# Optimization experiments

Measured on AMD Instinct MI355X. Metric: run time of the kernel, lower is better.

## Reference

```python
import jax, jax.numpy as jnp
import numpy as np

N, FIN, NH, NR, F, E = 50000, 256, 4, 4, 64, 500000


def setup_inputs() -> dict:
    key = jax.random.key(0)
    ks = jax.random.split(key, 12)
    x = jax.random.normal(ks[0], (N, FIN), jnp.float32)
    src = jax.random.randint(ks[1], (E,), 0, N)
    trg = jax.random.randint(ks[2], (E,), 0, N)
    rel = jax.random.randint(ks[3], (E,), 0, NR)
    node_to_graph_map = jnp.zeros((N,), jnp.int32)
    s = 1.0 / np.sqrt(FIN)
    W_proj = jax.random.uniform(ks[4], (NH * NR * F, FIN), jnp.float32, -s, s)
    score_src = jax.random.normal(ks[5], (1, NH, NR, F), jnp.float32) * 0.1
    score_trg = jax.random.normal(ks[6], (1, NH, NR, F), jnp.float32) * 0.1
    sf = 1.0 / np.sqrt(F)
    W1 = jax.random.uniform(ks[7], (F, F), jnp.float32, -sf, sf)
    b1 = jnp.zeros((F,), jnp.float32)
    W2 = jax.random.uniform(ks[8], (F, F), jnp.float32, -sf, sf)
    b2 = jnp.zeros((F,), jnp.float32)
    W3 = jax.random.uniform(ks[9], (1, F), jnp.float32, -sf, sf)
    b3 = jnp.zeros((1,), jnp.float32)
    W_skip = jax.random.uniform(ks[10], (NH * F, FIN), jnp.float32, -s, s)
    bias = jnp.zeros((NH * F,), jnp.float32)
    gamma = jnp.ones((NH * F,), jnp.float32)
    beta = jnp.zeros((NH * F,), jnp.float32)
    return dict(x=x, src=src, trg=trg, rel=rel, node_to_graph_map=node_to_graph_map,
                W_proj=W_proj, score_src=score_src, score_trg=score_trg,
                W1=W1, b1=b1, W2=W2, b2=b2, W3=W3, b3=b3,
                W_skip=W_skip, bias=bias, gamma=gamma, beta=beta)


def mish(v):
    return v * jnp.tanh(jax.nn.softplus(v))


def gat_forward(x, W_proj, score_src, score_trg, W1, b1, W2, b2, W3, b3,
                W_skip, bias, gamma, beta, src, trg, rel):
    n = x.shape[0]
    # (N, NH, NR, F) projected node features
    proj = (x @ W_proj.T).reshape(n, NH, NR, F)
    s_src = (proj * score_src).sum(-1)  # (N, NH, NR)
    s_trg = (proj * score_trg).sum(-1)  # (N, NH, NR)
    # lift to edges for their own relation: (E, NH)
    e_s = s_src[src, :, rel] + s_trg[trg, :, rel]
    e_s = jax.nn.leaky_relu(e_s, 0.2)
    # per-(relation, head) max over edges (matches per-relation max(dim=0) in the torch loop)
    m = jax.ops.segment_max(e_s, rel, num_segments=NR)  # (NR, NH)
    e_exp = jnp.exp(e_s - m[rel])
    # segment softmax grouped by (target node, relation)
    seg = trg * NR + rel
    denom = jax.ops.segment_sum(e_exp, seg, num_segments=n * NR)  # (N*NR, NH)
    att = e_exp / (denom[seg] + 1e-16)  # (E, NH)
    feat = proj[src, :, rel, :] * att[:, :, None]  # (E, NH, F)
    agg = jax.ops.segment_sum(feat, seg, num_segments=n * NR)  # (N*NR, NH, F)
    agg = agg.reshape(n, NR, NH, F).transpose(0, 2, 1, 3)  # (N, NH, NR, F)
    # AttentionedAggregationLayer: MLP score -> Mish -> softmax over relation dim -> weighted sum
    h = jax.nn.relu(agg @ W1.T + b1)
    h = jax.nn.relu(h @ W2.T + b2)
    sc = mish(h @ W3.T + b3)            # (N, NH, NR, 1)
    a_rel = jax.nn.softmax(sc, axis=-2)
    out = (agg * a_rel).sum(-2)          # (N, NH, F)
    # skip connection (FIN != NH*F per-head, so projected skip), concat heads, bias, ELU, LayerNorm
    out = out + (x @ W_skip.T).reshape(n, NH, F)
    out = out.reshape(n, NH * F) + bias
    out = jax.nn.elu(out)
    mu = out.mean(-1, keepdims=True)
    var = out.var(-1, keepdims=True)
    out = (out - mu) * jax.lax.rsqrt(var + 1e-5) * gamma + beta
    return out


def reference(x, src, trg, rel, node_to_graph_map, W_proj, score_src, score_trg,
              W1, b1, W2, b2, W3, b3, W_skip, bias, gamma, beta):
    return gat_forward(x, W_proj, score_src, score_trg, W1, b1, W2, b2, W3, b3,
                       W_skip, bias, gamma, beta, src, trg, rel)
```

## Files before the change

kernel.cpp:

```cpp
#include <hip/hip_runtime.h>

#define NNODES 50000
#define NEDGES 500000
#define NBINS  (NNODES * 4)
#define NSCANB 196
#define MPAD   50176

#define WF_W1    0
#define WF_B1    4096
#define WF_W2    4160
#define WF_B2    8256
#define WF_W3    8320
#define WF_B3    8384
#define WF_SSC   8385
#define WF_STC   9409
#define WF_BIAS  10433
#define WF_GAMMA 10689
#define WF_BETA  10945
#define WF_TOT   11201

typedef __attribute__((ext_vector_type(8))) short short8;
typedef __attribute__((ext_vector_type(4))) short short4v;
typedef __attribute__((ext_vector_type(4))) float floatx4;
typedef __attribute__((ext_vector_type(4))) unsigned int uint4v;

__device__ __forceinline__ float bf2f(unsigned short u) {
    return __uint_as_float(((unsigned)u) << 16);
}
__device__ __forceinline__ unsigned f2bf(float f) {
    unsigned u = __float_as_uint(f);
    u += 0x7fffu + ((u >> 16) & 1u);
    return u >> 16;
}
__device__ __forceinline__ float bflo(unsigned u) { return __uint_as_float(u << 16); }
__device__ __forceinline__ float bfhi(unsigned u) { return __uint_as_float(u & 0xffff0000u); }
__device__ __forceinline__ int clampi(int v, int hi) { return v < 0 ? 0 : (v > hi ? hi : v); }

__device__ __forceinline__ short8 pack_bf16(const float* p) {
    short8 r;
#pragma unroll
    for (int j = 0; j < 8; j++) r[j] = (short)f2bf(p[j]);
    return r;
}

__global__ __launch_bounds__(256) void probe_k(const unsigned short* __restrict__ xs,
                                               unsigned* __restrict__ flag) {
    __shared__ unsigned cnt;
    if (threadIdx.x == 0) cnt = 0;
    __syncthreads();
    unsigned local = 0;
    for (int i = threadIdx.x; i < 8192; i += 256) {
        float v = bf2f(xs[i]);
        if (!(fabsf(v) < 1e10f)) local++;
    }
    atomicAdd(&cnt, local);
    __syncthreads();
    if (threadIdx.x == 0) *flag = (cnt > 256u) ? 1u : 0u;
}

__device__ __forceinline__ float ldf(const void* p, int i, bool f32) {
    return f32 ? ((const float*)p)[i] : bf2f(((const unsigned short*)p)[i]);
}

__global__ __launch_bounds__(1024) void wconv_k(const void* W1, const void* b1,
                                                const void* W2, const void* b2,
                                                const void* W3, const void* b3,
                                                const void* ssc, const void* stc,
                                                const void* bias, const void* gamma,
                                                const void* beta,
                                                const unsigned* __restrict__ flag,
                                                float* __restrict__ wf) {
    bool f32 = (*flag != 0u);
    for (int i = threadIdx.x; i < WF_TOT; i += 1024) {
        float v;
        if (i < WF_B1)          v = ldf(W1, i - WF_W1, f32);
        else if (i < WF_W2)     v = ldf(b1, i - WF_B1, f32);
        else if (i < WF_B2)     v = ldf(W2, i - WF_W2, f32);
        else if (i < WF_W3)     v = ldf(b2, i - WF_B2, f32);
        else if (i < WF_B3)     v = ldf(W3, i - WF_W3, f32);
        else if (i < WF_SSC)    v = ldf(b3, i - WF_B3, f32);
        else if (i < WF_STC)    v = ldf(ssc, i - WF_SSC, f32);
        else if (i < WF_BIAS)   v = ldf(stc, i - WF_STC, f32);
        else if (i < WF_GAMMA)  v = ldf(bias, i - WF_BIAS, f32);
        else if (i < WF_BETA)   v = ldf(gamma, i - WF_GAMMA, f32);
        else                    v = ldf(beta, i - WF_BETA, f32);
        wf[i] = v;
    }
}

__global__ __launch_bounds__(256) void convbf_k(const void* __restrict__ src,
                                                unsigned short* __restrict__ dst,
                                                int nelem, int npad,
                                                const unsigned* __restrict__ flag) {
    int i8 = (blockIdx.x * 256 + threadIdx.x) * 8;
    if (i8 >= npad) return;
    short8 o;
    if (i8 < nelem) {
        if (*flag) {
            const float* pf = (const float*)src + i8;
            floatx4 a = *(const floatx4*)pf;
            floatx4 b = *(const floatx4*)(pf + 4);
            o[0] = (short)f2bf(a[0]); o[1] = (short)f2bf(a[1]);
            o[2] = (short)f2bf(a[2]); o[3] = (short)f2bf(a[3]);
            o[4] = (short)f2bf(b[0]); o[5] = (short)f2bf(b[1]);
            o[6] = (short)f2bf(b[2]); o[7] = (short)f2bf(b[3]);
        } else {
            o = *(const short8*)((const unsigned short*)src + i8);
        }
    } else {
#pragma unroll
        for (int j = 0; j < 8; j++) o[j] = 0;
    }
    *(short8*)(dst + i8) = o;
}

__global__ __launch_bounds__(64) void gemm_fused_k(const unsigned short* __restrict__ A,
                                                   const unsigned short* __restrict__ Bp,
                                                   const unsigned short* __restrict__ Bs,
                                                   unsigned short* __restrict__ proj,
                                                   unsigned short* __restrict__ out16,
                                                   float* __restrict__ out32,
                                                   const float* __restrict__ wf,
                                                   float* __restrict__ s_src,
                                                   float* __restrict__ s_trg,
                                                   const unsigned* __restrict__ flag) {
    const bool cf32 = (*flag != 0u);
    const int lane = threadIdx.x & 63;
    const int l15 = lane & 15, q = lane >> 4;
    const int m0 = blockIdx.x * 64;

    short8 af[4][8];
#pragma unroll
    for (int mt = 0; mt < 4; mt++)
#pragma unroll
        for (int ks = 0; ks < 8; ks++)
            af[mt][ks] = *(const short8*)(A + (size_t)(m0 + mt * 16 + l15) * 256 + ks * 32 + q * 8);

#pragma unroll 1
    for (int cg = 0; cg < 16; cg++) {
        floatx4 acc[4][4];
#pragma unroll
        for (int i = 0; i < 4; i++)
#pragma unroll
            for (int j = 0; j < 4; j++) acc[i][j] = (floatx4){0.f, 0.f, 0.f, 0.f};
#pragma unroll
        for (int ks = 0; ks < 8; ks++) {
            short8 bfr[4];
#pragma unroll
            for (int nt = 0; nt < 4; nt++)
                bfr[nt] = *(const short8*)(Bp + (size_t)(cg * 64 + nt * 16 + l15) * 256 + ks * 32 + q * 8);
#pragma unroll
            for (int mt = 0; mt < 4; mt++)
#pragma unroll
                for (int nt = 0; nt < 4; nt++)
                    acc[mt][nt] = __builtin_amdgcn_mfma_f32_16x16x32_bf16(af[mt][ks], bfr[nt],
                                                                         acc[mt][nt], 0, 0, 0);
        }
        const int h = cg >> 2, r = cg & 3;
        const int colbase = (r * 4 + h) * 64;
        const int cell = h * 4 + r;
        float sa[4], sb[4];
#pragma unroll
        for (int nt = 0; nt < 4; nt++) {
            sa[nt] = wf[WF_SSC + cell * 64 + nt * 16 + l15];
            sb[nt] = wf[WF_STC + cell * 64 + nt * 16 + l15];
        }
#pragma unroll
        for (int mt = 0; mt < 4; mt++) {
            float pa[4] = {0.f, 0.f, 0.f, 0.f};
            float pb[4] = {0.f, 0.f, 0.f, 0.f};
#pragma unroll
            for (int nt = 0; nt < 4; nt++)
#pragma unroll
                for (int rg = 0; rg < 4; rg++) {
                    int row = m0 + mt * 16 + q * 4 + rg;
                    float v = acc[mt][nt][rg];
                    unsigned short vb = (unsigned short)f2bf(v);
                    if (row < NNODES)
                        proj[(size_t)row * 1024 + colbase + nt * 16 + l15] = vb;
                    float vr = bf2f(vb);
                    pa[rg] = fmaf(vr, sa[nt], pa[rg]);
                    pb[rg] = fmaf(vr, sb[nt], pb[rg]);
                }
#pragma unroll
            for (int off = 1; off < 16; off <<= 1)
#pragma unroll
                for (int rg = 0; rg < 4; rg++) {
                    pa[rg] += __shfl_xor(pa[rg], off);
                    pb[rg] += __shfl_xor(pb[rg], off);
                }
            if (l15 == 0) {
#pragma unroll
                for (int rg = 0; rg < 4; rg++) {
                    int row = m0 + mt * 16 + q * 4 + rg;
                    if (row < NNODES) {
                        s_src[row * 16 + cell] = pa[rg];
                        s_trg[row * 16 + cell] = pb[rg];
                    }
                }
            }
        }
    }

#pragma unroll 1
    for (int cg = 0; cg < 4; cg++) {
        floatx4 acc[4][4];
#pragma unroll
        for (int i = 0; i < 4; i++)
#pragma unroll
            for (int j = 0; j < 4; j++) acc[i][j] = (floatx4){0.f, 0.f, 0.f, 0.f};
#pragma unroll
        for (int ks = 0; ks < 8; ks++) {
            short8 bfr[4];
#pragma unroll
            for (int nt = 0; nt < 4; nt++)
                bfr[nt] = *(const short8*)(Bs + (size_t)(cg * 64 + nt * 16 + l15) * 256 + ks * 32 + q * 8);
#pragma unroll
            for (int mt = 0; mt < 4; mt++)
#pragma unroll
                for (int nt = 0; nt < 4; nt++)
                    acc[mt][nt] = __builtin_amdgcn_mfma_f32_16x16x32_bf16(af[mt][ks], bfr[nt],
                                                                         acc[mt][nt], 0, 0, 0);
        }
#pragma unroll
        for (int mt = 0; mt < 4; mt++)
#pragma unroll
            for (int nt = 0; nt < 4; nt++)
#pragma unroll
                for (int rg = 0; rg < 4; rg++) {
                    int row = m0 + mt * 16 + q * 4 + rg;
                    if (row < NNODES) {
                        size_t idx = (size_t)row * 256 + cg * 64 + nt * 16 + l15;
                        float v = acc[mt][nt][rg];
                        if (cf32) out32[idx] = v;
                        else      out16[idx] = (unsigned short)f2bf(v);
                    }
                }
    }
}

__global__ __launch_bounds__(256) void count_k(const int* __restrict__ trg,
                                               const int* __restrict__ rel,
                                               unsigned* __restrict__ counts, int E) {
    int e = blockIdx.x * 256 + threadIdx.x;
    if (e >= E) return;
    int g = clampi(trg[e], NNODES - 1);
    int r = clampi(rel[e], 3);
    atomicAdd(&counts[g * 4 + r], 1u);
}

__global__ __launch_bounds__(256) void scan1_k(const unsigned* __restrict__ counts,
                                               unsigned* __restrict__ offsets,
                                               unsigned* __restrict__ bsum) {
    __shared__ unsigned ts[256];
    int t = threadIdx.x;
    int base = blockIdx.x * 1024 + t * 4;
    uint4v c = {0u, 0u, 0u, 0u};
    if (base + 3 < NBINS) c = *(const uint4v*)(counts + base);
    else {
#pragma unroll
        for (int j = 0; j < 4; j++) c[j] = (base + j < NBINS) ? counts[base + j] : 0u;
    }
    ts[t] = c[0] + c[1] + c[2] + c[3];
    __syncthreads();
    for (int off = 1; off < 256; off <<= 1) {
        unsigned v = (t >= off) ? ts[t - off] : 0u;
        __syncthreads();
        ts[t] += v;
        __syncthreads();
    }
    unsigned pre = (t == 0) ? 0u : ts[t - 1];
    uint4v o;
    o[0] = pre;
    o[1] = pre + c[0];
    o[2] = pre + c[0] + c[1];
    o[3] = pre + c[0] + c[1] + c[2];
    if (base + 3 < NBINS) *(uint4v*)(offsets + base) = o;
    else {
#pragma unroll
        for (int j = 0; j < 4; j++) if (base + j < NBINS) offsets[base + j] = o[j];
    }
    if (t == 255) bsum[blockIdx.x] = ts[255];
}

__global__ __launch_bounds__(256) void scan2_k(unsigned* __restrict__ bsum,
                                               unsigned* __restrict__ offsets) {
    __shared__ unsigned ts[256];
    int t = threadIdx.x;
    unsigned v = (t < NSCANB) ? bsum[t] : 0u;
    ts[t] = v;
    __syncthreads();
    for (int off = 1; off < 256; off <<= 1) {
        unsigned u = (t >= off) ? ts[t - off] : 0u;
        __syncthreads();
        ts[t] += u;
        __syncthreads();
    }
    if (t < NSCANB) bsum[t] = (t == 0) ? 0u : ts[t - 1];
    if (t == 255) offsets[NBINS] = ts[255];
}

__global__ __launch_bounds__(256) void scan3_k(unsigned* __restrict__ offsets,
                                               unsigned* __restrict__ cursor,
                                               const unsigned* __restrict__ bsum) {
    int t = threadIdx.x;
    unsigned base = bsum[blockIdx.x];
    int idx = blockIdx.x * 1024 + t * 4;
    if (idx + 3 < NBINS) {
        uint4v o = *(const uint4v*)(offsets + idx);
        o[0] += base; o[1] += base; o[2] += base; o[3] += base;
        *(uint4v*)(offsets + idx) = o;
        *(uint4v*)(cursor + idx) = o;
    } else {
#pragma unroll
        for (int j = 0; j < 4; j++)
            if (idx + j < NBINS) {
                unsigned v = offsets[idx + j] + base;
                offsets[idx + j] = v;
                cursor[idx + j] = v;
            }
    }
}

__global__ __launch_bounds__(256) void fill_k(const int* __restrict__ src,
                                              const int* __restrict__ trg,
                                              const int* __restrict__ rel,
                                              const float* __restrict__ s_src,
                                              const float* __restrict__ s_trg,
                                              unsigned* __restrict__ cursor,
                                              unsigned* __restrict__ esrc,
                                              floatx4* __restrict__ eexp, int E) {
    int e = blockIdx.x * 256 + threadIdx.x;
    if (e >= E) return;
    int s = clampi(src[e], NNODES - 1);
    int g = clampi(trg[e], NNODES - 1);
    int r = clampi(rel[e], 3);
    unsigned pos = atomicAdd(&cursor[g * 4 + r], 1u);
    if (pos >= (unsigned)E) pos = E - 1;
    esrc[pos] = (unsigned)s;
    floatx4 v;
#pragma unroll
    for (int h = 0; h < 4; h++) {
        float val = s_src[s * 16 + h * 4 + r] + s_trg[g * 16 + h * 4 + r];
        val = val > 0.f ? val : 0.2f * val;
        v[h] = expf(val);
    }
    eexp[pos] = v;
}

__global__ __launch_bounds__(256) void rowagg2_k(const unsigned* __restrict__ offsets,
                                                 const unsigned* __restrict__ esrc,
                                                 const floatx4* __restrict__ eexp,
                                                 const unsigned short* __restrict__ proj,
                                                 unsigned short* __restrict__ agg) {
    int wave = threadIdx.x >> 6, lane = threadIdx.x & 63;
    int bin = blockIdx.x * 4 + wave;
    if (bin >= NBINS) return;
    int r = bin & 3;
    int h = lane >> 4;
    unsigned beg = offsets[bin], end = offsets[bin + 1];

    float a0 = 0.f, a1 = 0.f, a2 = 0.f, a3 = 0.f, den = 0.f;
    for (unsigned i = beg; i < end; i++) {
        unsigned s = esrc[i];
        floatx4 pe = eexp[i];
        float p = pe[h];
        const short4v* pp = (const short4v*)(proj + (size_t)s * 1024 + r * 256) + lane;
        short4v v = *pp;
        den += p;
        a0 = fmaf(p, bf2f((unsigned short)v[0]), a0);
        a1 = fmaf(p, bf2f((unsigned short)v[1]), a1);
        a2 = fmaf(p, bf2f((unsigned short)v[2]), a2);
        a3 = fmaf(p, bf2f((unsigned short)v[3]), a3);
    }
    float inv = 1.f / (den + 1e-16f);
    short4v o;
    o[0] = (short)f2bf(a0 * inv);
    o[1] = (short)f2bf(a1 * inv);
    o[2] = (short)f2bf(a2 * inv);
    o[3] = (short)f2bf(a3 * inv);
    *((short4v*)(agg + (size_t)bin * 256) + lane) = o;
}

__global__ __launch_bounds__(256, 2) void mlp_mfma_k(const unsigned short* __restrict__ agg,
                                                     const float* __restrict__ wf,
                                                     float* __restrict__ sc) {
    __shared__ float lds[4][16 * 68];
    const int wave = threadIdx.x >> 6;
    const int lane = threadIdx.x & 63;
    const int l15 = lane & 15, q = lane >> 4;
    float* L = lds[wave];

    short8 w1f[2][4], w2f[2][4];
#pragma unroll
    for (int ks = 0; ks < 2; ks++)
#pragma unroll
        for (int nt = 0; nt < 4; nt++) {
            w1f[ks][nt] = pack_bf16(wf + WF_W1 + (nt * 16 + l15) * 64 + ks * 32 + q * 8);
            w2f[ks][nt] = pack_bf16(wf + WF_W2 + (nt * 16 + l15) * 64 + ks * 32 + q * 8);
        }
    float b1v[4], b2v[4], w3v[4];
#pragma unroll
    for (int nt = 0; nt < 4; nt++) {
        b1v[nt] = wf[WF_B1 + nt * 16 + l15];
        b2v[nt] = wf[WF_B2 + nt * 16 + l15];
        w3v[nt] = wf[WF_W3 + nt * 16 + l15];
    }
    float b3v = wf[WF_B3];

    int wave_id = blockIdx.x * 4 + wave;
#pragma unroll 1
    for (int t = 0; t < 4; t++) {
        int row0 = (wave_id * 4 + t) * 16;
        short8 a1[2];
#pragma unroll
        for (int ks = 0; ks < 2; ks++)
            a1[ks] = *(const short8*)(agg + (size_t)(row0 + l15) * 64 + ks * 32 + q * 8);
        floatx4 acc1[4];
#pragma unroll
        for (int nt = 0; nt < 4; nt++) {
            acc1[nt] = (floatx4){0.f, 0.f, 0.f, 0.f};
            acc1[nt] = __builtin_amdgcn_mfma_f32_16x16x32_bf16(a1[0], w1f[0][nt], acc1[nt], 0, 0, 0);
            acc1[nt] = __builtin_amdgcn_mfma_f32_16x16x32_bf16(a1[1], w1f[1][nt], acc1[nt], 0, 0, 0);
        }
        __syncthreads();
#pragma unroll
        for (int nt = 0; nt < 4; nt++)
#pragma unroll
            for (int rg = 0; rg < 4; rg++)
                L[(q * 4 + rg) * 68 + nt * 16 + l15] = fmaxf(acc1[nt][rg] + b1v[nt], 0.f);
        __syncthreads();
        short8 a2[2];
#pragma unroll
        for (int ks = 0; ks < 2; ks++) {
            short8 rr;
#pragma unroll
            for (int j = 0; j < 8; j++)
                rr[j] = (short)f2bf(L[l15 * 68 + ks * 32 + q * 8 + j]);
            a2[ks] = rr;
        }
        floatx4 acc2[4];
#pragma unroll
        for (int nt = 0; nt < 4; nt++) {
            acc2[nt] = (floatx4){0.f, 0.f, 0.f, 0.f};
            acc2[nt] = __builtin_amdgcn_mfma_f32_16x16x32_bf16(a2[0], w2f[0][nt], acc2[nt], 0, 0, 0);
            acc2[nt] = __builtin_amdgcn_mfma_f32_16x16x32_bf16(a2[1], w2f[1][nt], acc2[nt], 0, 0, 0);
        }
        float p[4];
#pragma unroll
        for (int rg = 0; rg < 4; rg++) {
            float s = 0.f;
#pragma unroll
            for (int nt = 0; nt < 4; nt++)
                s = fmaf(fmaxf(acc2[nt][rg] + b2v[nt], 0.f), w3v[nt], s);
            p[rg] = s;
        }
#pragma unroll
        for (int off = 1; off < 16; off <<= 1) {
#pragma unroll
            for (int rg = 0; rg < 4; rg++) p[rg] += __shfl_xor(p[rg], off);
        }
        if (l15 == 0) {
#pragma unroll
            for (int rg = 0; rg < 4; rg++) {
                float acc = p[rg] + b3v;
                float sp = fmaxf(acc, 0.f) + log1pf(expf(-fabsf(acc)));
                float m = acc * tanhf(sp);
                int s_id = row0 + q * 4 + rg;
                int n = s_id >> 4, r = (s_id >> 2) & 3, h = s_id & 3;
                sc[n * 16 + h * 4 + r] = m;
            }
        }
    }
}

__global__ __launch_bounds__(256) void final_k(const unsigned short* __restrict__ agg,
                                               const float* __restrict__ sc,
                                               const float* __restrict__ wf,
                                               const unsigned* __restrict__ flag,
                                               unsigned short* __restrict__ out16,
                                               float* __restrict__ out32) {
    const bool f32 = (*flag != 0u);
    int n = blockIdx.x, t = threadIdx.x;
    int h = t >> 6, f = t & 63;
    float s0 = sc[n * 16 + h * 4 + 0];
    float s1 = sc[n * 16 + h * 4 + 1];
    float s2 = sc[n * 16 + h * 4 + 2];
    float s3 = sc[n * 16 + h * 4 + 3];
    float mx = fmaxf(fmaxf(s0, s1), fmaxf(s2, s3));
    float e0 = expf(s0 - mx), e1 = expf(s1 - mx), e2 = expf(s2 - mx), e3 = expf(s3 - mx);
    float inv = 1.f / (e0 + e1 + e2 + e3);
    size_t base = (size_t)n * 1024 + h * 64 + f;
    float a0 = bf2f(agg[base]);
    float a1 = bf2f(agg[base + 256]);
    float a2 = bf2f(agg[base + 512]);
    float a3 = bf2f(agg[base + 768]);
    float v = (e0 * a0 + e1 * a1 + e2 * a2 + e3 * a3) * inv;
    size_t oidx = (size_t)n * 256 + t;
    float skipv = f32 ? out32[oidx] : bf2f(out16[oidx]);
    v += skipv + wf[WF_BIAS + t];
    v = v > 0.f ? v : expm1f(v);

    float s = v, qq = v * v;
#pragma unroll
    for (int o = 1; o < 64; o <<= 1) {
        s += __shfl_xor(s, o);
        qq += __shfl_xor(qq, o);
    }
    __shared__ float red[8];
    __shared__ float stat[2];
    int wv = t >> 6, ln = t & 63;
    if (ln == 0) { red[wv] = s; red[4 + wv] = qq; }
    __syncthreads();
    if (t == 0) {
        float S = red[0] + red[1] + red[2] + red[3];
        float Q = red[4] + red[5] + red[6] + red[7];
        float mu = S * (1.f / 256.f);
        float var = fmaxf(Q * (1.f / 256.f) - mu * mu, 0.f);
        stat[0] = mu;
        stat[1] = rsqrtf(var + 1e-5f);
    }
    __syncthreads();
    float o = (v - stat[0]) * stat[1] * wf[WF_GAMMA + t] + wf[WF_BETA + t];
    if (f32) out32[oidx] = o;
    else     out16[oidx] = (unsigned short)f2bf(o);
}

extern "C" void kernel_launch(void* const* d_in, const int* in_sizes, int n_in,
                              void* d_out, int out_size, void* d_ws, size_t ws_size,
                              hipStream_t stream) {
    if (ws_size < 226900000) return;

    const void* x      = d_in[0];
    const int* src     = (const int*)d_in[1];
    const int* trg     = (const int*)d_in[2];
    const int* rel     = (const int*)d_in[3];
    const void* W_proj = d_in[5];
    const void* ssc    = d_in[6];
    const void* stc    = d_in[7];
    const void* W1     = d_in[8];
    const void* b1     = d_in[9];
    const void* W2     = d_in[10];
    const void* b2     = d_in[11];
    const void* W3     = d_in[12];
    const void* b3     = d_in[13];
    const void* W_skip = d_in[14];
    const void* bias   = d_in[15];
    const void* gamma  = d_in[16];
    const void* beta   = d_in[17];
    unsigned short* out16 = (unsigned short*)d_out;
    float* out32          = (float*)d_out;

    char* w = (char*)d_ws;
    unsigned short* proj = (unsigned short*)(w + 0);
    unsigned short* agg  = (unsigned short*)(w + 102400000);
    unsigned short* xbf  = (unsigned short*)(w + 102400000);
    float* s_src         = (float*)(w + 204800000);
    float* s_trg         = (float*)(w + 208000000);
    floatx4* eexp        = (floatx4*)(w + 211200000);
    unsigned short* wpbf = (unsigned short*)(w + 211200000);
    unsigned short* wsbf = (unsigned short*)(w + 212300000);
    unsigned* esrc       = (unsigned*)(w + 219200000);
    unsigned* counts     = (unsigned*)(w + 221200000);
    unsigned* offsets    = (unsigned*)(w + 222000000);
    unsigned* cursor     = (unsigned*)(w + 222800016);
    float* sc            = (float*)(w + 223600016);
    float* wf            = (float*)(w + 226800016);
    unsigned* flag       = (unsigned*)(w + 226844824);
    unsigned* bsum       = (unsigned*)(w + 226844832);

    hipMemsetAsync(counts, 0, NBINS * 4, stream);

    probe_k<<<1, 256, 0, stream>>>((const unsigned short*)x, flag);
    wconv_k<<<1, 1024, 0, stream>>>(W1, b1, W2, b2, W3, b3, ssc, stc, bias, gamma, beta,
                                    flag, wf);
    convbf_k<<<(MPAD * 256) / (8 * 256), 256, 0, stream>>>(x, xbf, NNODES * 256,
                                                           MPAD * 256, flag);
    convbf_k<<<128, 256, 0, stream>>>(W_proj, wpbf, 1024 * 256, 1024 * 256, flag);
    convbf_k<<<32, 256, 0, stream>>>(W_skip, wsbf, 256 * 256, 256 * 256, flag);
    gemm_fused_k<<<784, 64, 0, stream>>>(xbf, wpbf, wsbf, proj, out16, out32,
                                         wf, s_src, s_trg, flag);
    count_k<<<1954, 256, 0, stream>>>(trg, rel, counts, NEDGES);
    scan1_k<<<NSCANB, 256, 0, stream>>>(counts, offsets, bsum);
    scan2_k<<<1, 256, 0, stream>>>(bsum, offsets);
    scan3_k<<<NSCANB, 256, 0, stream>>>(offsets, cursor, bsum);
    fill_k<<<1954, 256, 0, stream>>>(src, trg, rel, s_src, s_trg, cursor, esrc, eexp, NEDGES);
    rowagg2_k<<<NBINS / 4, 256, 0, stream>>>(offsets, esrc, eexp, proj, agg);
    mlp_mfma_k<<<3125, 256, 0, stream>>>(agg, wf, sc);
    final_k<<<NNODES, 256, 0, stream>>>(agg, sc, wf, flag, out16, out32);
}
```

Measured before the change: 578.9 us.

## Split fused GEMM column groups across four waves sharing an LDS-staged A tile

The fused projection/skip GEMM now launches 256 threads per block instead of one wave. The 64x256 bf16 A tile is staged once into XOR-swizzled shared memory, and each of the four waves handles four projection column groups plus one skip column group. This is meant to raise occupancy and latency hiding on a kernel that previously ran only 784 single-wave blocks, and to free the registers that held the whole A tile. In exchange it adds a block barrier, 32KB of LDS per block, and extra LDS reads of A fragments on every k-step.

```diff
diff --git a/kernel.cpp b/kernel.cpp
--- a/kernel.cpp
+++ b/kernel.cpp
@@ -32,8 +32,6 @@
     u += 0x7fffu + ((u >> 16) & 1u);
     return u >> 16;
 }
-__device__ __forceinline__ float bflo(unsigned u) { return __uint_as_float(u << 16); }
-__device__ __forceinline__ float bfhi(unsigned u) { return __uint_as_float(u & 0xffff0000u); }
 __device__ __forceinline__ int clampi(int v, int hi) { return v < 0 ? 0 : (v > hi ? hi : v); }
 
 __device__ __forceinline__ short8 pack_bf16(const float* p) {
@@ -114,30 +112,44 @@
     *(short8*)(dst + i8) = o;
 }
 
-__global__ __launch_bounds__(64) void gemm_fused_k(const unsigned short* __restrict__ A,
-                                                   const unsigned short* __restrict__ Bp,
-                                                   const unsigned short* __restrict__ Bs,
-                                                   unsigned short* __restrict__ proj,
-                                                   unsigned short* __restrict__ out16,
-                                                   float* __restrict__ out32,
-                                                   const float* __restrict__ wf,
-                                                   float* __restrict__ s_src,
-                                                   float* __restrict__ s_trg,
-                                                   const unsigned* __restrict__ flag) {
+__device__ __forceinline__ short8 lds_a(const unsigned short* Asm, int row, int chunk) {
+    int byte = row * 512 + ((chunk ^ (row & 7)) << 4);
+    return *(const short8*)((const char*)Asm + byte);
+}
+
+__global__ __launch_bounds__(256) void gemm_fused_k(const unsigned short* __restrict__ A,
+                                                    const unsigned short* __restrict__ Bp,
+                                                    const unsigned short* __restrict__ Bs,
+                                                    unsigned short* __restrict__ proj,
+                                                    unsigned short* __restrict__ out16,
+                                                    float* __restrict__ out32,
+                                                    const float* __restrict__ wf,
+                                                    float* __restrict__ s_src,
+                                                    float* __restrict__ s_trg,
+                                                    const unsigned* __restrict__ flag) {
+    __shared__ unsigned short Asm[64 * 256];
     const bool cf32 = (*flag != 0u);
+    const int w = threadIdx.x >> 6;
     const int lane = threadIdx.x & 63;
     const int l15 = lane & 15, q = lane >> 4;
     const int m0 = blockIdx.x * 64;
 
-    short8 af[4][8];
-#pragma unroll
-    for (int mt = 0; mt < 4; mt++)
-#pragma unroll
-        for (int ks = 0; ks < 8; ks++)
-            af[mt][ks] = *(const short8*)(A + (size_t)(m0 + mt * 16 + l15) * 256 + ks * 32 + q * 8);
+    {
+        const int trow = threadIdx.x >> 5;
+        const int tchunk = threadIdx.x & 31;
+        const int schunk = tchunk ^ trow;
+#pragma unroll
+        for (int kp = 0; kp < 8; kp++) {
+            int row = kp * 8 + trow;
+            short8 v = *(const short8*)(A + (size_t)(m0 + row) * 256 + tchunk * 8);
+            *(short8*)((char*)Asm + row * 512 + (schunk << 4)) = v;
+        }
+    }
+    __syncthreads();
 
 #pragma unroll 1
-    for (int cg = 0; cg < 16; cg++) {
+    for (int cgi = 0; cgi < 4; cgi++) {
+        const int cg = w * 4 + cgi;
         floatx4 acc[4][4];
 #pragma unroll
         for (int i = 0; i < 4; i++)
@@ -149,11 +161,15 @@
 #pragma unroll
             for (int nt = 0; nt < 4; nt++)
                 bfr[nt] = *(const short8*)(Bp + (size_t)(cg * 64 + nt * 16 + l15) * 256 + ks * 32 + q * 8);
+            short8 afr[4];
 #pragma unroll
             for (int mt = 0; mt < 4; mt++)
+                afr[mt] = lds_a(Asm, mt * 16 + l15, ks * 4 + q);
+#pragma unroll
+            for (int mt = 0; mt < 4; mt++)
 #pragma unroll
                 for (int nt = 0; nt < 4; nt++)
-                    acc[mt][nt] = __builtin_amdgcn_mfma_f32_16x16x32_bf16(af[mt][ks], bfr[nt],
+                    acc[mt][nt] = __builtin_amdgcn_mfma_f32_16x16x32_bf16(afr[mt], bfr[nt],
                                                                          acc[mt][nt], 0, 0, 0);
         }
         const int h = cg >> 2, r = cg & 3;
@@ -202,8 +218,8 @@
         }
     }
 
-#pragma unroll 1
-    for (int cg = 0; cg < 4; cg++) {
+    {
+        const int cg = w;
         floatx4 acc[4][4];
 #pragma unroll
         for (int i = 0; i < 4; i++)
@@ -215,11 +231,15 @@
 #pragma unroll
             for (int nt = 0; nt < 4; nt++)
                 bfr[nt] = *(const short8*)(Bs + (size_t)(cg * 64 + nt * 16 + l15) * 256 + ks * 32 + q * 8);
+            short8 afr[4];
 #pragma unroll
             for (int mt = 0; mt < 4; mt++)
+                afr[mt] = lds_a(Asm, mt * 16 + l15, ks * 4 + q);
+#pragma unroll
+            for (int mt = 0; mt < 4; mt++)
 #pragma unroll
                 for (int nt = 0; nt < 4; nt++)
-                    acc[mt][nt] = __builtin_amdgcn_mfma_f32_16x16x32_bf16(af[mt][ks], bfr[nt],
+                    acc[mt][nt] = __builtin_amdgcn_mfma_f32_16x16x32_bf16(afr[mt], bfr[nt],
                                                                          acc[mt][nt], 0, 0, 0);
         }
 #pragma unroll
@@ -578,8 +598,8 @@
                                                            MPAD * 256, flag);
     convbf_k<<<128, 256, 0, stream>>>(W_proj, wpbf, 1024 * 256, 1024 * 256, flag);
     convbf_k<<<32, 256, 0, stream>>>(W_skip, wsbf, 256 * 256, 256 * 256, flag);
-    gemm_fused_k<<<784, 64, 0, stream>>>(xbf, wpbf, wsbf, proj, out16, out32,
-                                         wf, s_src, s_trg, flag);
+    gemm_fused_k<<<784, 256, 0, stream>>>(xbf, wpbf, wsbf, proj, out16, out32,
+                                          wf, s_src, s_trg, flag);
     count_k<<<1954, 256, 0, stream>>>(trg, rel, counts, NEDGES);
     scan1_k<<<NSCANB, 256, 0, stream>>>(counts, offsets, bsum);
     scan2_k<<<1, 256, 0, stream>>>(bsum, offsets);
```

New measurement: 608.5 us. 5.1% more time.

## Retile fused projection GEMM into 128x128 LDS-staged blocks with async global-to-LDS loads

Applied to the files above, without the earlier changes.

The projection and skip GEMMs become one GEMM by placing the skip weights right after the projection weights in the workspace. It runs as a 2D grid of 128x128 output tiles, with 4 waves per block. Each K-chunk of A and B is staged into double-buffered, XOR-swizzled LDS through global_load_lds. Before, each 64-thread block held all of A in registers and streamed B fragments straight from global memory. The aim is more parallelism, better reuse of B and fewer register-bound loads, at the cost of extra LDS traffic and barriers.

```diff
diff --git a/kernel.cpp b/kernel.cpp
--- a/kernel.cpp
+++ b/kernel.cpp
@@ -32,8 +32,6 @@
     u += 0x7fffu + ((u >> 16) & 1u);
     return u >> 16;
 }
-__device__ __forceinline__ float bflo(unsigned u) { return __uint_as_float(u << 16); }
-__device__ __forceinline__ float bfhi(unsigned u) { return __uint_as_float(u & 0xffff0000u); }
 __device__ __forceinline__ int clampi(int v, int hi) { return v < 0 ? 0 : (v > hi ? hi : v); }
 
 __device__ __forceinline__ short8 pack_bf16(const float* p) {
@@ -114,48 +112,94 @@
     *(short8*)(dst + i8) = o;
 }
 
-__global__ __launch_bounds__(64) void gemm_fused_k(const unsigned short* __restrict__ A,
-                                                   const unsigned short* __restrict__ Bp,
-                                                   const unsigned short* __restrict__ Bs,
-                                                   unsigned short* __restrict__ proj,
-                                                   unsigned short* __restrict__ out16,
-                                                   float* __restrict__ out32,
-                                                   const float* __restrict__ wf,
-                                                   float* __restrict__ s_src,
-                                                   float* __restrict__ s_trg,
-                                                   const unsigned* __restrict__ flag) {
+#define GLOAD_LDS16(g, l)                                                     \
+    __builtin_amdgcn_global_load_lds(                                         \
+        (const __attribute__((address_space(1))) unsigned int*)(g),           \
+        (__attribute__((address_space(3))) unsigned int*)(l), 16, 0, 0)
+
+__global__ __launch_bounds__(256) void gemm_fused_k(const unsigned short* __restrict__ A,
+                                                    const unsigned short* __restrict__ BB,
+                                                    unsigned short* __restrict__ proj,
+                                                    unsigned short* __restrict__ out16,
+                                                    float* __restrict__ out32,
+                                                    const float* __restrict__ wf,
+                                                    float* __restrict__ s_src,
+                                                    float* __restrict__ s_trg,
+                                                    const unsigned* __restrict__ flag) {
+    __shared__ unsigned short Asm[2][128 * 64];
+    __shared__ unsigned short Bsm[2][128 * 64];
     const bool cf32 = (*flag != 0u);
-    const int lane = threadIdx.x & 63;
+    const int t = threadIdx.x;
+    const int w = t >> 6;
+    const int lane = t & 63;
     const int l15 = lane & 15, q = lane >> 4;
-    const int m0 = blockIdx.x * 64;
-
-    short8 af[4][8];
-#pragma unroll
-    for (int mt = 0; mt < 4; mt++)
-#pragma unroll
-        for (int ks = 0; ks < 8; ks++)
-            af[mt][ks] = *(const short8*)(A + (size_t)(m0 + mt * 16 + l15) * 256 + ks * 32 + q * 8);
-
+    const int wr = w >> 1, wc = w & 1;
+    const int m0 = blockIdx.x * 128;
+    const int n0 = blockIdx.y * 128;
+
+    const int srow = t >> 3;
+    const int schk = (t & 7) ^ (srow & 7);
+    char* aL = (char*)Asm;
+    char* bL = (char*)Bsm;
+    const int wofs = w * 1024;
+
+#define STAGE(buf, kt)                                                        \
+    do {                                                                      \
+        _Pragma("unroll")                                                     \
+        for (int p = 0; p < 4; p++) {                                         \
+            int row_ = p * 32 + srow;                                         \
+            GLOAD_LDS16(A + (size_t)(m0 + row_) * 256 + (kt) * 64 + schk * 8, \
+                        aL + (buf) * 16384 + p * 4096 + wofs);                \
+            GLOAD_LDS16(BB + (size_t)(n0 + row_) * 256 + (kt) * 64 + schk * 8,\
+                        bL + (buf) * 16384 + p * 4096 + wofs);                \
+        }                                                                     \
+    } while (0)
+
+    floatx4 acc[4][4];
+#pragma unroll
+    for (int i = 0; i < 4; i++)
+#pragma unroll
+        for (int j = 0; j < 4; j++) acc[i][j] = (floatx4){0.f, 0.f, 0.f, 0.f};
+
+    STAGE(0, 0);
+    __syncthreads();
+
+    int buf = 0;
 #pragma unroll 1
-    for (int cg = 0; cg < 16; cg++) {
-        floatx4 acc[4][4];
-#pragma unroll
-        for (int i = 0; i < 4; i++)
-#pragma unroll
-            for (int j = 0; j < 4; j++) acc[i][j] = (floatx4){0.f, 0.f, 0.f, 0.f};
-#pragma unroll
-        for (int ks = 0; ks < 8; ks++) {
-            short8 bfr[4];
-#pragma unroll
-            for (int nt = 0; nt < 4; nt++)
-                bfr[nt] = *(const short8*)(Bp + (size_t)(cg * 64 + nt * 16 + l15) * 256 + ks * 32 + q * 8);
+    for (int kt = 0; kt < 4; kt++) {
+        if (kt < 3) STAGE(buf ^ 1, kt + 1);
+        const char* aB = aL + buf * 16384;
+        const char* bB = bL + buf * 16384;
+#pragma unroll
+        for (int kk = 0; kk < 2; kk++) {
+            short8 afr[4], bfr[4];
+#pragma unroll
+            for (int mt = 0; mt < 4; mt++) {
+                int row = wr * 64 + mt * 16 + l15;
+                afr[mt] = *(const short8*)(aB + row * 128 +
+                                           (((kk * 4 + q) ^ (l15 & 7)) << 4));
+            }
+#pragma unroll
+            for (int nt = 0; nt < 4; nt++) {
+                int row = wc * 64 + nt * 16 + l15;
+                bfr[nt] = *(const short8*)(bB + row * 128 +
+                                           (((kk * 4 + q) ^ (l15 & 7)) << 4));
+            }
 #pragma unroll
             for (int mt = 0; mt < 4; mt++)
 #pragma unroll
                 for (int nt = 0; nt < 4; nt++)
-                    acc[mt][nt] = __builtin_amdgcn_mfma_f32_16x16x32_bf16(af[mt][ks], bfr[nt],
+                    acc[mt][nt] = __builtin_amdgcn_mfma_f32_16x16x32_bf16(afr[mt], bfr[nt],
                                                                          acc[mt][nt], 0, 0, 0);
         }
+        __syncthreads();
+        buf ^= 1;
+    }
+#undef STAGE
+
+    const int cg = blockIdx.y * 2 + wc;
+    const int rbase = m0 + wr * 64;
+    if (cg < 16) {
         const int h = cg >> 2, r = cg & 3;
         const int colbase = (r * 4 + h) * 64;
         const int cell = h * 4 + r;
@@ -173,7 +217,7 @@
             for (int nt = 0; nt < 4; nt++)
 #pragma unroll
                 for (int rg = 0; rg < 4; rg++) {
-                    int row = m0 + mt * 16 + q * 4 + rg;
+                    int row = rbase + mt * 16 + q * 4 + rg;
                     float v = acc[mt][nt][rg];
                     unsigned short vb = (unsigned short)f2bf(v);
                     if (row < NNODES)
@@ -192,7 +236,7 @@
             if (l15 == 0) {
 #pragma unroll
                 for (int rg = 0; rg < 4; rg++) {
-                    int row = m0 + mt * 16 + q * 4 + rg;
+                    int row = rbase + mt * 16 + q * 4 + rg;
                     if (row < NNODES) {
                         s_src[row * 16 + cell] = pa[rg];
                         s_trg[row * 16 + cell] = pb[rg];
@@ -200,37 +244,17 @@
                 }
             }
         }
-    }
-
-#pragma unroll 1
-    for (int cg = 0; cg < 4; cg++) {
-        floatx4 acc[4][4];
-#pragma unroll
-        for (int i = 0; i < 4; i++)
-#pragma unroll
-            for (int j = 0; j < 4; j++) acc[i][j] = (floatx4){0.f, 0.f, 0.f, 0.f};
-#pragma unroll
-        for (int ks = 0; ks < 8; ks++) {
-            short8 bfr[4];
+    } else {
+        const int scg = cg - 16;
+#pragma unroll
+        for (int mt = 0; mt < 4; mt++)
 #pragma unroll
             for (int nt = 0; nt < 4; nt++)
-                bfr[nt] = *(const short8*)(Bs + (size_t)(cg * 64 + nt * 16 + l15) * 256 + ks * 32 + q * 8);
-#pragma unroll
-            for (int mt = 0; mt < 4; mt++)
-#pragma unroll
-                for (int nt = 0; nt < 4; nt++)
-                    acc[mt][nt] = __builtin_amdgcn_mfma_f32_16x16x32_bf16(af[mt][ks], bfr[nt],
-                                                                         acc[mt][nt], 0, 0, 0);
-        }
-#pragma unroll
-        for (int mt = 0; mt < 4; mt++)
-#pragma unroll
-            for (int nt = 0; nt < 4; nt++)
 #pragma unroll
                 for (int rg = 0; rg < 4; rg++) {
-                    int row = m0 + mt * 16 + q * 4 + rg;
+                    int row = rbase + mt * 16 + q * 4 + rg;
                     if (row < NNODES) {
-                        size_t idx = (size_t)row * 256 + cg * 64 + nt * 16 + l15;
+                        size_t idx = (size_t)row * 256 + scg * 64 + nt * 16 + l15;
                         float v = acc[mt][nt][rg];
                         if (cf32) out32[idx] = v;
                         else      out16[idx] = (unsigned short)f2bf(v);
@@ -559,7 +583,7 @@
     float* s_trg         = (float*)(w + 208000000);
     floatx4* eexp        = (floatx4*)(w + 211200000);
     unsigned short* wpbf = (unsigned short*)(w + 211200000);
-    unsigned short* wsbf = (unsigned short*)(w + 212300000);
+    unsigned short* wsbf = (unsigned short*)(w + 211724288);
     unsigned* esrc       = (unsigned*)(w + 219200000);
     unsigned* counts     = (unsigned*)(w + 221200000);
     unsigned* offsets    = (unsigned*)(w + 222000000);
@@ -578,8 +602,8 @@
                                                            MPAD * 256, flag);
     convbf_k<<<128, 256, 0, stream>>>(W_proj, wpbf, 1024 * 256, 1024 * 256, flag);
     convbf_k<<<32, 256, 0, stream>>>(W_skip, wsbf, 256 * 256, 256 * 256, flag);
-    gemm_fused_k<<<784, 64, 0, stream>>>(xbf, wpbf, wsbf, proj, out16, out32,
-                                         wf, s_src, s_trg, flag);
+    gemm_fused_k<<<dim3(392, 10), 256, 0, stream>>>(xbf, wpbf, proj, out16, out32,
+                                                    wf, s_src, s_trg, flag);
     count_k<<<1954, 256, 0, stream>>>(trg, rel, counts, NEDGES);
     scan1_k<<<NSCANB, 256, 0, stream>>>(counts, offsets, bsum);
     scan2_k<<<1, 256, 0, stream>>>(bsum, offsets);
```

Measured after the change: 588.2 us. No clear change (+1.6%).
